# Optimization experiments

Measured on AMD Instinct MI355X. Metric: run time of the kernel, lower is better.

Reference implementation:

```python
import jax, jax.numpy as jnp
import numpy as np

B, T, C = 4, 2048, 1024
NH = 16
HD = C // NH  # 64


def setup_inputs() -> dict:
    key = jax.random.key(0)
    k1, k2, k3 = jax.random.split(key, 3)
    x = jax.random.normal(k1, (B, T, C), dtype=jnp.float32)
    # causal mask buffer, 1 = keep, 0 = mask out
    mask = jnp.tril(jnp.ones((T, T), dtype=jnp.int32))[None, None, :, :]
    # learned params (Linear with bias=False): torch stores weight as [out, in],
    # y = x @ W.T ; we store transposed for direct matmul
    w_qkv = jax.random.normal(k2, (C, 3 * C), dtype=jnp.float32) / np.sqrt(C)
    w_proj = jax.random.normal(k3, (C, C), dtype=jnp.float32) / np.sqrt(C)
    return {"x": x, "mask": mask, "w_qkv": w_qkv, "w_proj": w_proj}


def reference(x, mask, w_qkv, w_proj):
    b, t, c = x.shape
    qkv = x @ w_qkv  # [b, t, 3c]
    q, k, v = jnp.split(qkv, 3, axis=-1)
    # [b, nh, t, hd]
    q = q.reshape(b, t, NH, HD).transpose(0, 2, 1, 3)
    k = k.reshape(b, t, NH, HD).transpose(0, 2, 1, 3)
    v = v.reshape(b, t, NH, HD).transpose(0, 2, 1, 3)
    att = jnp.einsum("bhqd,bhkd->bhqk", q, k) * (1.0 / np.sqrt(HD))
    att = jnp.where(mask == 0, -jnp.inf, att)
    att = jax.nn.softmax(att, axis=-1)
    y = jnp.einsum("bhqk,bhkd->bhqd", att, v)
    y = y.transpose(0, 2, 1, 3).reshape(b, t, c)
    return y @ w_proj
```

## Files before the change

### kernel.cpp

```cpp
#include <hip/hip_runtime.h>
#include <hip/hip_bf16.h>

typedef _Float16 f16;
typedef __attribute__((ext_vector_type(4))) _Float16 f16x4;
typedef __attribute__((ext_vector_type(8))) _Float16 f16x8;
typedef __attribute__((ext_vector_type(4))) float f32x4;

#define MFMA16(a, b, c) __builtin_amdgcn_mfma_f32_16x16x16f16((a), (b), (c), 0, 0, 0)
#define MFMA32(a, b, c) __builtin_amdgcn_mfma_f32_16x16x32_f16((a), (b), (c), 0, 0, 0)
#define EXP2(x) __builtin_amdgcn_exp2f(x)
#define GLOAD_LDS16(g, l)                                                        \
  __builtin_amdgcn_global_load_lds((const __attribute__((address_space(1))) void*)(g), \
                                   (__attribute__((address_space(3))) void*)(l), 16, 0, 0)
typedef const __attribute__((address_space(3))) char* lds_cp;
#define TR16(dst, addr, imm) \
  asm volatile("ds_read_b64_tr_b16 %0, %1 offset:" imm : "=v"(dst) : "v"(addr))

__global__ __launch_bounds__(256) void cast_f32_f16_kernel(
    const float* __restrict__ in, f16* __restrict__ out, int n4) {
  int i = blockIdx.x * 256 + threadIdx.x;
  if (i >= n4) return;
  const float4 v = reinterpret_cast<const float4*>(in)[i];
  f16x4 h;
  h[0] = (f16)v.x; h[1] = (f16)v.y; h[2] = (f16)v.z; h[3] = (f16)v.w;
  reinterpret_cast<f16x4*>(out)[i] = h;
}

__global__ __launch_bounds__(256) void transpose_cast_kernel(
    const float* __restrict__ src, f16* __restrict__ dst, int R, int Cc) {
  __shared__ float t[32][33];
  int tx0 = blockIdx.x * 32, ty0 = blockIdx.y * 32;
  int c = threadIdx.x & 31;
  int r0 = threadIdx.x >> 5;
#pragma unroll
  for (int i = 0; i < 4; i++) {
    int r = r0 + 8 * i;
    t[r][c] = src[(size_t)(ty0 + r) * Cc + tx0 + c];
  }
  __syncthreads();
#pragma unroll
  for (int i = 0; i < 4; i++) {
    int a = r0 + 8 * i;
    dst[(size_t)(tx0 + a) * R + ty0 + c] = (f16)t[c][a];
  }
}

template <bool OUT_F32>
__global__ __launch_bounds__(256) void gemm_f16_kernel(
    const f16* __restrict__ A, const f16* __restrict__ Bt, void* __restrict__ Cout,
    int M, int N, int K) {
  constexpr int BK = 32;
  __shared__ f16 Al[3][128 * BK];
  __shared__ f16 Bl[3][128 * BK];

  const int tid = threadIdx.x;
  const int lane = tid & 63, wid = tid >> 6;
  const int wm = wid >> 1, wn = wid & 1;
  const int lo = lane & 15, hi = lane >> 4;
  const int tn0 = blockIdx.x * 128, tm0 = blockIdx.y * 128;

  f32x4 acc[4][4] = {};

  const int r1 = tid >> 2, o1 = (tid & 3) * 8;

  auto stage = [&](int kt, int c) {
    GLOAD_LDS16(&A[(size_t)(tm0 + r1) * K + kt + o1], &Al[c][tid * 8]);
    GLOAD_LDS16(&A[(size_t)(tm0 + r1 + 64) * K + kt + o1], &Al[c][(tid + 256) * 8]);
    GLOAD_LDS16(&Bt[(size_t)(tn0 + r1) * K + kt + o1], &Bl[c][tid * 8]);
    GLOAD_LDS16(&Bt[(size_t)(tn0 + r1 + 64) * K + kt + o1], &Bl[c][(tid + 256) * 8]);
  };

  auto compute = [&](int cur) {
    f16x8 af[4], bf[4];
#pragma unroll
    for (int mi = 0; mi < 4; mi++)
      af[mi] = *(const f16x8*)&Al[cur][(wm * 64 + mi * 16 + lo) * BK + 8 * hi];
#pragma unroll
    for (int ni = 0; ni < 4; ni++)
      bf[ni] = *(const f16x8*)&Bl[cur][(wn * 64 + ni * 16 + lo) * BK + 8 * hi];
    __builtin_amdgcn_s_setprio(1);
#pragma unroll
    for (int mi = 0; mi < 4; mi++)
#pragma unroll
      for (int ni = 0; ni < 4; ni++)
        acc[mi][ni] = MFMA32(af[mi], bf[ni], acc[mi][ni]);
    __builtin_amdgcn_s_setprio(0);
  };

  const int NT = K / BK;
  stage(0, 0);
  stage(BK, 1);

  int cur = 0;
  for (int t = 0; t < NT - 1; t++) {
    asm volatile("s_waitcnt vmcnt(4)" ::: "memory");
    __builtin_amdgcn_s_barrier();
    if (t + 2 < NT) stage((t + 2) * BK, (t + 2) % 3);
    compute(cur);
    cur = (cur == 2) ? 0 : cur + 1;
  }
  asm volatile("s_waitcnt vmcnt(0)" ::: "memory");
  __builtin_amdgcn_s_barrier();
  compute(cur);

#pragma unroll
  for (int mi = 0; mi < 4; mi++)
#pragma unroll
    for (int ni = 0; ni < 4; ni++)
#pragma unroll
      for (int r = 0; r < 4; r++) {
        int row = tm0 + wm * 64 + mi * 16 + 4 * hi + r;
        int col = tn0 + wn * 64 + ni * 16 + lo;
        float v = acc[mi][ni][r];
        if (OUT_F32)
          ((float*)Cout)[(size_t)row * N + col] = v;
        else
          ((f16*)Cout)[(size_t)row * N + col] = (f16)v;
      }
}

__global__ __launch_bounds__(256, 4) void attn_kernel(
    const f16* __restrict__ qkv, f16* __restrict__ y) {
  constexpr int T = 2048, NHD = 3072, LDO = 72;
  const int bh = blockIdx.x;
  const int b = bh >> 4, h = bh & 15;
  const int pr = blockIdx.y;
  const int tid = threadIdx.x;
  const int lane = tid & 63, w = tid >> 6;
  const int lo = lane & 15, hi = lane >> 4;

  const size_t base = (size_t)b * T * NHD + (size_t)h * 64;
  const f16* Qp = qkv + base;
  const f16* Kp = qkv + base + 1024;
  const f16* Vp = qkv + base + 2048;

  __shared__ __align__(16) char smem[32768];
  f16 (*Ol)[LDO] = (f16(*)[LDO])smem;

  const int tile[2] = {pr, 31 - pr};
  const int qb[2] = {tile[0] * 64 + w * 16, tile[1] * 64 + w * 16};

  const float scf = 0.125f * 1.44269504089f;
  f16x8 qf[2][2];
#pragma unroll
  for (int s = 0; s < 2; s++) {
    const f16* qrow = Qp + (size_t)(qb[s] + lo) * NHD;
#pragma unroll
    for (int ks = 0; ks < 2; ks++) {
      f16x8 v = *(const f16x8*)&qrow[ks * 32 + 8 * hi];
#pragma unroll
      for (int j = 0; j < 8; j++) v[j] = (f16)((float)v[j] * scf);
      qf[s][ks] = v;
    }
  }

  f32x4 oacc[2][4] = {};
  float mreg[2] = {-1e30f, -1e30f};
  float lsum[2] = {0.f, 0.f};

  const int kr = tid >> 3;
  const int kslot = (tid & 7) ^ (kr & 7);
  const int tp = tid & 127;
  const int vkey = 4 * (tp >> 3) + ((tp >> 1) & 3);
  const int vcol = (tid >> 7) * 16 + (tid & 1) * 8;

  const int kfo0 = lo * 64 + ((hi ^ (lo & 7)) * 8);
  const int kfo1 = lo * 64 + (((4 + hi) ^ (lo & 7)) * 8);

  auto stage = [&](int kv, int c) {
    char* kb = smem + c * 8192;
    char* vb = smem + 16384 + c * 8192;
    GLOAD_LDS16(&Kp[(size_t)(kv + kr) * NHD + kslot * 8], kb + tid * 16);
    GLOAD_LDS16(&Kp[(size_t)(kv + kr + 32) * NHD + kslot * 8], kb + 4096 + tid * 16);
    GLOAD_LDS16(&Vp[(size_t)(kv + vkey) * NHD + vcol], vb + tid * 16);
    GLOAD_LDS16(&Vp[(size_t)(kv + vkey) * NHD + vcol + 32], vb + 4096 + tid * 16);
  };

  const int nt = 32 - pr;
  stage(0, 0);
  asm volatile("s_waitcnt vmcnt(0)" ::: "memory");
  __builtin_amdgcn_s_barrier();

  for (int t = 0; t < nt; t++) {
    const int cur = t & 1;
    const int kv0 = t * 64;
    if (t + 1 < nt) stage(kv0 + 64, cur ^ 1);

    const f16* Kl = (const f16*)(smem + cur * 8192);
    const bool act0 = kv0 <= qb[0] + 15;

    f16x8 kf[2][4];
#pragma unroll
    for (int ct = 0; ct < 4; ct++) {
      kf[0][ct] = *(const f16x8*)&Kl[ct * 1024 + kfo0];
      kf[1][ct] = *(const f16x8*)&Kl[ct * 1024 + kfo1];
    }

    f16x4 pb[2][4];
#pragma unroll
    for (int s = 0; s < 2; s++) {
      if (s == 0 && !act0) continue;
      f32x4 s_[4] = {};
      __builtin_amdgcn_s_setprio(1);
#pragma unroll
      for (int ks = 0; ks < 2; ks++)
#pragma unroll
        for (int ct = 0; ct < 4; ct++)
          s_[ct] = MFMA32(kf[ks][ct], qf[s][ks], s_[ct]);
      __builtin_amdgcn_s_setprio(0);

      if (kv0 + 63 > qb[s]) {
        const int q = qb[s] + lo;
#pragma unroll
        for (int ct = 0; ct < 4; ct++)
#pragma unroll
          for (int r = 0; r < 4; r++)
            if (kv0 + ct * 16 + 4 * hi + r > q) s_[ct][r] = -3.0e38f;
      }
      float mt = -3.0e38f;
#pragma unroll
      for (int ct = 0; ct < 4; ct++)
        mt = fmaxf(mt, fmaxf(fmaxf(s_[ct][0], s_[ct][1]), fmaxf(s_[ct][2], s_[ct][3])));
      mt = fmaxf(mt, __shfl_xor(mt, 16));
      mt = fmaxf(mt, __shfl_xor(mt, 32));
      float mn = mreg[s];
      if (!__all(mt <= mn + 8.f)) {
        mn = fmaxf(mn, mt);
        const float al = EXP2(mreg[s] - mn);
        mreg[s] = mn;
        lsum[s] *= al;
#pragma unroll
        for (int ct = 0; ct < 4; ct++)
#pragma unroll
          for (int r = 0; r < 4; r++) oacc[s][ct][r] *= al;
      }
      float rs = 0.f;
#pragma unroll
      for (int ct = 0; ct < 4; ct++)
#pragma unroll
        for (int r = 0; r < 4; r++) {
          float p = EXP2(s_[ct][r] - mn);
          rs += p;
          pb[s][ct][r] = (f16)p;
        }
      rs += __shfl_xor(rs, 16);
      rs += __shfl_xor(rs, 32);
      lsum[s] += rs;
    }

    lds_cp vtrb = (lds_cp)(smem + 16384 + cur * 8192) + lane * 8;
#pragma unroll
    for (int ct = 0; ct < 4; ct++) {
      lds_cp bct = vtrb + ct * 2048;
      f16x4 v0, v1, v2, v3;
      TR16(v0, bct, "0");
      TR16(v1, bct, "512");
      TR16(v2, bct, "1024");
      TR16(v3, bct, "1536");
      asm volatile("s_waitcnt lgkmcnt(0)" ::: "memory");
      __builtin_amdgcn_sched_barrier(0);
      __builtin_amdgcn_s_setprio(1);
      if (act0) {
        oacc[0][ct] = MFMA16(v0, pb[0][0], oacc[0][ct]);
        oacc[0][ct] = MFMA16(v1, pb[0][1], oacc[0][ct]);
        oacc[0][ct] = MFMA16(v2, pb[0][2], oacc[0][ct]);
        oacc[0][ct] = MFMA16(v3, pb[0][3], oacc[0][ct]);
      }
      oacc[1][ct] = MFMA16(v0, pb[1][0], oacc[1][ct]);
      oacc[1][ct] = MFMA16(v1, pb[1][1], oacc[1][ct]);
      oacc[1][ct] = MFMA16(v2, pb[1][2], oacc[1][ct]);
      oacc[1][ct] = MFMA16(v3, pb[1][3], oacc[1][ct]);
      __builtin_amdgcn_s_setprio(0);
    }

    asm volatile("s_waitcnt vmcnt(0)" ::: "memory");
    __builtin_amdgcn_s_barrier();
  }

#pragma unroll
  for (int s = 0; s < 2; s++) {
    __syncthreads();
    const float inv = 1.f / lsum[s];
#pragma unroll
    for (int ct = 0; ct < 4; ct++) {
      f16x4 o4;
#pragma unroll
      for (int r = 0; r < 4; r++) o4[r] = (f16)(oacc[s][ct][r] * inv);
      *(f16x4*)&Ol[w * 16 + lo][ct * 16 + 4 * hi] = o4;
    }
    __syncthreads();
#pragma unroll
    for (int i = 0; i < 2; i++) {
      int idx = tid + 256 * i;
      int qq = idx >> 3, ch = idx & 7;
      *(f16x8*)&y[((size_t)b * T + tile[s] * 64 + qq) * 1024 + (size_t)h * 64 + ch * 8] =
          *(const f16x8*)&Ol[qq][ch * 8];
    }
  }
}

extern "C" void kernel_launch(void* const* d_in, const int* in_sizes, int n_in,
                              void* d_out, int out_size, void* d_ws, size_t ws_size,
                              hipStream_t stream) {
  const float* x = (const float*)d_in[0];
  const float* w_qkv = (const float*)d_in[2];
  const float* w_proj = (const float*)d_in[3];

  constexpr int B = 4, T = 2048, C = 1024, NH = 16;
  constexpr int M = B * T;
  constexpr int N1 = 3 * C;

  char* ws = (char*)d_ws;
  f16* x16 = (f16*)ws;    ws += (size_t)M * C * 2;
  f16* wqkvT = (f16*)ws;  ws += (size_t)N1 * C * 2;
  f16* wprojT = (f16*)ws; ws += (size_t)C * C * 2;
  f16* qkvb = (f16*)ws;   ws += (size_t)M * N1 * 2;
  f16* y16 = (f16*)ws;

  cast_f32_f16_kernel<<<(M * C / 4 + 255) / 256, 256, 0, stream>>>(x, x16, M * C / 4);
  transpose_cast_kernel<<<dim3(N1 / 32, C / 32), 256, 0, stream>>>(w_qkv, wqkvT, C, N1);
  transpose_cast_kernel<<<dim3(C / 32, C / 32), 256, 0, stream>>>(w_proj, wprojT, C, C);
  gemm_f16_kernel<false><<<dim3(N1 / 128, M / 128), 256, 0, stream>>>(x16, wqkvT, qkvb, M, N1, C);
  attn_kernel<<<dim3(B * NH, 16), 256, 0, stream>>>(qkvb, y16);
  gemm_f16_kernel<true><<<dim3(C / 128, M / 128), 256, 0, stream>>>(y16, wprojT, (float*)d_out, M, C, C);
}
```

Before: 179.7 us.

## Replace QKV GEMM with 256x256-tile, 512-thread phased-pipeline kernel

Adds a new QKV projection GEMM with 256x256 output tiles per 512-thread workgroup. It double-buffers 128 KB of LDS using direct global-to-LDS loads, XOR-swizzles the LDS layout, and splits each 64-wide k-tile into phases that interleave staging with MFMA bursts at raised priority. Workgroup IDs are remapped so neighbouring blocks share data in cache. The goal is higher arithmetic intensity and better overlap of memory with compute than the 128x128 kernel. In exchange it uses very large LDS and many registers per workgroup, and its barrier-heavy schedule is fragile.

```diff
diff --git a/kernel.cpp b/kernel.cpp
--- a/kernel.cpp
+++ b/kernel.cpp
@@ -43,6 +43,145 @@
     int a = r0 + 8 * i;
     dst[(size_t)(tx0 + a) * R + ty0 + c] = (f16)t[c][a];
   }
+}
+
+__global__ __launch_bounds__(512, 2) void gemm256_8ph_kernel(
+    const f16* __restrict__ A, const f16* __restrict__ Bt, f16* __restrict__ C,
+    int M, int N, int K) {
+  __shared__ __align__(16) char smem[131072];
+  const int tid = threadIdx.x;
+  const int lane = tid & 63, wid = tid >> 6;
+  const int wm = wid >> 2, wn = wid & 3;
+  const int lo = lane & 15, hi = lane >> 4;
+
+  const int ntn = N >> 8;
+  const int nwg = (M >> 8) * ntn;
+  const int wg = (blockIdx.x & 7) * (nwg >> 3) + (blockIdx.x >> 3);
+  const int tm0 = (wg / ntn) << 8, tn0 = (wg % ntn) << 8;
+
+  const int sr = tid >> 3;
+  const int sc8 = (tid & 7) ^ (sr & 7);
+
+  const int sw = lo & 7;
+  const int aoff0 = wm * 16384 + lo * 128 + ((hi ^ sw) << 4);
+  const int aoff1 = wm * 16384 + lo * 128 + (((4 + hi) ^ sw) << 4);
+  const int brow = ((wn & 1) * 64 + lo) * 128;
+  const int boff0 = 32768 + (wn >> 1) * 16384 + brow + ((hi ^ sw) << 4);
+  const int boff1 = 32768 + (wn >> 1) * 16384 + brow + (((4 + hi) ^ sw) << 4);
+
+  f32x4 acc[8][4] = {};
+
+  const int nslots = K >> 4;
+  auto stage_slot = [&](int s) {
+    if (s >= nslots) return;
+    const int kt = s >> 2, ct = s & 3;
+    char* dst = smem + (kt & 1) * 65536 + ct * 16384 + tid * 16;
+    const f16* src = (ct < 2) ? (A + (size_t)(tm0 + (ct & 1) * 128) * K)
+                              : (Bt + (size_t)(tn0 + (ct & 1) * 128) * K);
+    const f16* p = src + (size_t)sr * K + kt * 64 + sc8 * 8;
+    GLOAD_LDS16(p, dst);
+    GLOAD_LDS16(p + ((size_t)K << 6), dst + 8192);
+  };
+
+  auto ktile4 = [&](const char* db, int sb) {
+    f16x8 a[4][2], bA[2][2], bB[2][2];
+    asm volatile("s_waitcnt vmcnt(2)" ::: "memory");
+    __builtin_amdgcn_s_barrier();
+#pragma unroll
+    for (int mi = 0; mi < 4; mi++) {
+      a[mi][0] = *(const f16x8*)(db + aoff0 + mi * 2048);
+      a[mi][1] = *(const f16x8*)(db + aoff1 + mi * 2048);
+    }
+#pragma unroll
+    for (int nn = 0; nn < 2; nn++) {
+      bA[nn][0] = *(const f16x8*)(db + boff0 + nn * 2048);
+      bA[nn][1] = *(const f16x8*)(db + boff1 + nn * 2048);
+    }
+    stage_slot(sb);
+    __builtin_amdgcn_s_barrier();
+    asm volatile("s_waitcnt lgkmcnt(0)" ::: "memory");
+    __builtin_amdgcn_sched_barrier(0);
+    __builtin_amdgcn_s_setprio(1);
+#pragma unroll
+    for (int mi = 0; mi < 4; mi++)
+#pragma unroll
+      for (int nn = 0; nn < 2; nn++) {
+        acc[mi][nn] = MFMA32(a[mi][0], bA[nn][0], acc[mi][nn]);
+        acc[mi][nn] = MFMA32(a[mi][1], bA[nn][1], acc[mi][nn]);
+      }
+    __builtin_amdgcn_s_setprio(0);
+    __builtin_amdgcn_s_barrier();
+#pragma unroll
+    for (int nn = 0; nn < 2; nn++) {
+      bB[nn][0] = *(const f16x8*)(db + boff0 + (2 + nn) * 2048);
+      bB[nn][1] = *(const f16x8*)(db + boff1 + (2 + nn) * 2048);
+    }
+    stage_slot(sb + 1);
+    __builtin_amdgcn_s_barrier();
+    asm volatile("s_waitcnt lgkmcnt(0)" ::: "memory");
+    __builtin_amdgcn_sched_barrier(0);
+    __builtin_amdgcn_s_setprio(1);
+#pragma unroll
+    for (int mi = 0; mi < 4; mi++)
+#pragma unroll
+      for (int nn = 0; nn < 2; nn++) {
+        acc[mi][2 + nn] = MFMA32(a[mi][0], bB[nn][0], acc[mi][2 + nn]);
+        acc[mi][2 + nn] = MFMA32(a[mi][1], bB[nn][1], acc[mi][2 + nn]);
+      }
+    __builtin_amdgcn_s_setprio(0);
+    __builtin_amdgcn_s_barrier();
+#pragma unroll
+    for (int mi = 0; mi < 4; mi++) {
+      a[mi][0] = *(const f16x8*)(db + aoff0 + 8192 + mi * 2048);
+      a[mi][1] = *(const f16x8*)(db + aoff1 + 8192 + mi * 2048);
+    }
+    stage_slot(sb + 2);
+    __builtin_amdgcn_s_barrier();
+    asm volatile("s_waitcnt lgkmcnt(0)" ::: "memory");
+    __builtin_amdgcn_sched_barrier(0);
+    __builtin_amdgcn_s_setprio(1);
+#pragma unroll
+    for (int mi = 0; mi < 4; mi++)
+#pragma unroll
+      for (int nn = 0; nn < 2; nn++) {
+        acc[4 + mi][nn] = MFMA32(a[mi][0], bA[nn][0], acc[4 + mi][nn]);
+        acc[4 + mi][nn] = MFMA32(a[mi][1], bA[nn][1], acc[4 + mi][nn]);
+      }
+    __builtin_amdgcn_s_setprio(0);
+    __builtin_amdgcn_s_barrier();
+    stage_slot(sb + 3);
+    __builtin_amdgcn_s_barrier();
+    __builtin_amdgcn_s_setprio(1);
+#pragma unroll
+    for (int mi = 0; mi < 4; mi++)
+#pragma unroll
+      for (int nn = 0; nn < 2; nn++) {
+        acc[4 + mi][2 + nn] = MFMA32(a[mi][0], bB[nn][0], acc[4 + mi][2 + nn]);
+        acc[4 + mi][2 + nn] = MFMA32(a[mi][1], bB[nn][1], acc[4 + mi][2 + nn]);
+      }
+    __builtin_amdgcn_s_setprio(0);
+  };
+
+  for (int s = 0; s < 5; s++) stage_slot(s);
+  asm volatile("s_waitcnt vmcnt(2)" ::: "memory");
+  __builtin_amdgcn_s_barrier();
+
+  const int NI = K >> 7;
+  for (int t = 0; t < NI; t++) {
+    ktile4(smem, 8 * t + 5);
+    ktile4(smem + 65536, 8 * t + 9);
+  }
+
+#pragma unroll
+  for (int mi = 0; mi < 8; mi++)
+#pragma unroll
+    for (int ni = 0; ni < 4; ni++)
+#pragma unroll
+      for (int r = 0; r < 4; r++) {
+        int row = tm0 + wm * 128 + mi * 16 + 4 * hi + r;
+        int col = tn0 + wn * 64 + ni * 16 + lo;
+        C[(size_t)row * N + col] = (f16)acc[mi][ni][r];
+      }
 }
 
 template <bool OUT_F32>
@@ -320,7 +459,7 @@
   cast_f32_f16_kernel<<<(M * C / 4 + 255) / 256, 256, 0, stream>>>(x, x16, M * C / 4);
   transpose_cast_kernel<<<dim3(N1 / 32, C / 32), 256, 0, stream>>>(w_qkv, wqkvT, C, N1);
   transpose_cast_kernel<<<dim3(C / 32, C / 32), 256, 0, stream>>>(w_proj, wprojT, C, C);
-  gemm_f16_kernel<false><<<dim3(N1 / 128, M / 128), 256, 0, stream>>>(x16, wqkvT, qkvb, M, N1, C);
+  gemm256_8ph_kernel<<<(M / 256) * (N1 / 256), 512, 0, stream>>>(x16, wqkvT, qkvb, M, N1, C);
   attn_kernel<<<dim3(B * NH, 16), 256, 0, stream>>>(qkvb, y16);
   gemm_f16_kernel<true><<<dim3(C / 128, M / 128), 256, 0, stream>>>(y16, wprojT, (float*)d_out, M, C, C);
 }
```

Result: faster. 175.8 us (-2.2%).

## Add 256x128-tile QKV GEMM with swizzled LDS and XCD-aware block remap

Applied to the files above, without the earlier changes.

Replaces the QKV projection GEMM with a new kernel that uses 256x128 output tiles, double-buffered direct global-to-LDS loads with an XOR-swizzled layout, and a block-index remap that spreads tiles across the 8 XCDs. Each wave computes 128x64 outputs with 16x16x32 MFMAs, so it reuses each loaded operand across more MFMAs. The larger tile and 128 accumulator registers per lane may lower occupancy. Only two LDS buffers are used, so there is less prefetch depth than the old triple-buffered kernel.

```diff
diff --git a/kernel.cpp b/kernel.cpp
--- a/kernel.cpp
+++ b/kernel.cpp
@@ -43,6 +43,88 @@
     int a = r0 + 8 * i;
     dst[(size_t)(tx0 + a) * R + ty0 + c] = (f16)t[c][a];
   }
+}
+
+__global__ __launch_bounds__(256, 3) void gemm_bt_kernel(
+    const f16* __restrict__ A, const f16* __restrict__ Bt, f16* __restrict__ C,
+    int M, int N, int K) {
+  __shared__ __align__(16) char smem[49152];
+  const int tid = threadIdx.x;
+  const int lane = tid & 63, wid = tid >> 6;
+  const int wm = wid >> 1, wn = wid & 1;
+  const int lo = lane & 15, hi = lane >> 4;
+
+  const int ntn = N >> 7;
+  const int nwg = (M >> 8) * ntn;
+  const int wg = (blockIdx.x & 7) * (nwg >> 3) + (blockIdx.x >> 3);
+  const int tm0 = (wg / ntn) << 8, tn0 = (wg % ntn) << 7;
+
+  const f16* asrc[4];
+  const f16* bsrc[2];
+#pragma unroll
+  for (int i = 0; i < 4; i++) {
+    int L = tid + 256 * i;
+    int prow = L >> 3, u = (L & 7) ^ (prow & 7);
+    int grow = prow * 2 + (u >> 2), gk8 = u & 3;
+    asrc[i] = A + (size_t)(tm0 + grow) * K + gk8 * 8;
+  }
+#pragma unroll
+  for (int i = 0; i < 2; i++) {
+    int L = tid + 256 * i;
+    int prow = L >> 3, u = (L & 7) ^ (prow & 7);
+    int grow = prow * 2 + (u >> 2), gk8 = u & 3;
+    bsrc[i] = Bt + (size_t)(tn0 + grow) * K + gk8 * 8;
+  }
+
+  const int slot = ((lo & 1) * 4 + hi) ^ ((lo >> 1) & 7);
+  const int abyte = (wm * 64 + (lo >> 1)) * 128 + slot * 16;
+  const int bbyte = 16384 + (wn * 32 + (lo >> 1)) * 128 + slot * 16;
+
+  f32x4 acc[8][4] = {};
+
+  auto stage = [&](int kt, char* buf) {
+#pragma unroll
+    for (int i = 0; i < 4; i++)
+      GLOAD_LDS16(asrc[i] + kt, buf + (tid + 256 * i) * 16);
+#pragma unroll
+    for (int i = 0; i < 2; i++)
+      GLOAD_LDS16(bsrc[i] + kt, buf + 16384 + (tid + 256 * i) * 16);
+  };
+
+  const int NT = K >> 5;
+  stage(0, smem);
+
+  for (int t = 0; t < NT; t++) {
+    char* db = smem + (t & 1) * 24576;
+    asm volatile("s_waitcnt vmcnt(0)" ::: "memory");
+    __builtin_amdgcn_s_barrier();
+    if (t + 1 < NT) stage((t + 1) * 32, smem + ((t + 1) & 1) * 24576);
+    __builtin_amdgcn_sched_barrier(0);
+
+    f16x8 a[8], b[4];
+#pragma unroll
+    for (int mi = 0; mi < 8; mi++) a[mi] = *(const f16x8*)(db + abyte + mi * 1024);
+#pragma unroll
+    for (int ni = 0; ni < 4; ni++) b[ni] = *(const f16x8*)(db + bbyte + ni * 1024);
+    __builtin_amdgcn_s_setprio(1);
+#pragma unroll
+    for (int mi = 0; mi < 8; mi++)
+#pragma unroll
+      for (int ni = 0; ni < 4; ni++)
+        acc[mi][ni] = MFMA32(a[mi], b[ni], acc[mi][ni]);
+    __builtin_amdgcn_s_setprio(0);
+  }
+
+#pragma unroll
+  for (int mi = 0; mi < 8; mi++)
+#pragma unroll
+    for (int ni = 0; ni < 4; ni++)
+#pragma unroll
+      for (int r = 0; r < 4; r++) {
+        int row = tm0 + wm * 128 + mi * 16 + 4 * hi + r;
+        int col = tn0 + wn * 64 + ni * 16 + lo;
+        C[(size_t)row * N + col] = (f16)acc[mi][ni][r];
+      }
 }
 
 template <bool OUT_F32>
@@ -320,7 +402,7 @@
   cast_f32_f16_kernel<<<(M * C / 4 + 255) / 256, 256, 0, stream>>>(x, x16, M * C / 4);
   transpose_cast_kernel<<<dim3(N1 / 32, C / 32), 256, 0, stream>>>(w_qkv, wqkvT, C, N1);
   transpose_cast_kernel<<<dim3(C / 32, C / 32), 256, 0, stream>>>(w_proj, wprojT, C, C);
-  gemm_f16_kernel<false><<<dim3(N1 / 128, M / 128), 256, 0, stream>>>(x16, wqkvT, qkvb, M, N1, C);
+  gemm_bt_kernel<<<(M / 256) * (N1 / 128), 256, 0, stream>>>(x16, wqkvT, qkvb, M, N1, C);
   attn_kernel<<<dim3(B * NH, 16), 256, 0, stream>>>(qkvb, y16);
   gemm_f16_kernel<true><<<dim3(C / 128, M / 128), 256, 0, stream>>>(y16, wprojT, (float*)d_out, M, C, C);
 }
```

Result: slower. 266.9 us (+48.5%).
